# Optimization experiments

Hardware: AMD Instinct MI355X
Metric: run time of the kernel (lower is better)

The kernel has to match this reference:

```python
import jax, jax.numpy as jnp
import numpy as np

K_BITS = 8
QMAX = float(2 ** (K_BITS - 1) - 1)  # 127 for symmetric int8 fake quant
BN_EPS = 1e-5
RES_SCALE = 1.0


def _ste(v, q):
    # straight-through estimator: forward q, backward identity wrt v
    return v + jax.lax.stop_gradient(q - v)


def quant_act(x, alpha):
    # PAMS-style: clamp to learnable alpha, symmetric uniform fake-quant
    xc = jnp.clip(x, -alpha, alpha)
    scale = alpha / QMAX
    q = jnp.round(xc / scale) * scale
    return _ste(xc, q)


def quant_weight(w):
    # symmetric max-abs weight fake-quant
    scale = jnp.max(jnp.abs(w)) / QMAX
    q = jnp.clip(jnp.round(w / scale), -QMAX, QMAX) * scale
    return _ste(w, q)


def conv3x3(x, w):
    return jax.lax.conv_general_dilated(
        x, w, window_strides=(1, 1), padding=[(1, 1), (1, 1)],
        dimension_numbers=("NCHW", "OIHW", "NCHW"))


def batchnorm(x, gamma, beta):
    # training-mode BN: biased batch statistics over (N, H, W)
    mean = jnp.mean(x, axis=(0, 2, 3), keepdims=True)
    var = jnp.var(x, axis=(0, 2, 3), keepdims=True)
    xhat = (x - mean) * jax.lax.rsqrt(var + BN_EPS)
    return xhat * gamma[None, :, None, None] + beta[None, :, None, None]


def prelu(x, a):
    return jnp.where(x >= 0, x, a * x)


def setup_inputs() -> dict:
    key = jax.random.key(0)
    ks = jax.random.split(key, 4)
    C = 64
    identity = jax.random.normal(ks[0], (8, C, 192, 192), dtype=jnp.float32)
    # conv weights, default_init_weights scale 0.1 (kaiming-ish * 0.1)
    w1 = jax.random.normal(ks[1], (C, C, 3, 3), dtype=jnp.float32) * 0.1
    w2 = jax.random.normal(ks[2], (C, C, 3, 3), dtype=jnp.float32) * 0.1
    return {
        "identity": identity,
        "bits": jnp.ones((1,), jnp.float32),
        "f": jnp.ones((1,), jnp.float32),
        "bits_out": jnp.zeros((1,), jnp.float32),
        "w1": w1,
        "w2": w2,
        "alpha1": jnp.array(8.0, jnp.float32),
        "alpha2": jnp.array(8.0, jnp.float32),
        "gamma1": jnp.ones((C,), jnp.float32),
        "beta1": jnp.zeros((C,), jnp.float32),
        "gamma2": jnp.ones((C,), jnp.float32),
        "beta2": jnp.zeros((C,), jnp.float32),
        "prelu_a": jnp.array(0.25, jnp.float32),
        "shortcut": jnp.ones((1,), jnp.float32),
    }


def reference(identity, bits, f, bits_out, w1, w2, alpha1, alpha2,
              gamma1, beta1, gamma2, beta2, prelu_a, shortcut):
    # quant conv1: quantize input act + weights, 3x3 conv
    x = conv3x3(quant_act(identity, alpha1), quant_weight(w1))
    # PReLU then BN1 (module applies bn1(act(x)))
    x = batchnorm(prelu(x, prelu_a), gamma1, beta1)
    # quant conv2
    out = conv3x3(quant_act(x, alpha2), quant_weight(w2))
    out = batchnorm(out, gamma2, beta2)
    out = identity * shortcut + out * RES_SCALE
    return (out, bits, f, bits_out)
```

## Files before the change

kernel.cpp:

```cpp
#include <hip/hip_runtime.h>
#include <hip/hip_bf16.h>
#include <math.h>

#define CNUM   64
#define HH     192
#define WW     192
#define NBATCH 8
#define HWSZ   (HH * WW)
#define CHWSZ  (CNUM * HWSZ)
#define TOTALSZ ((size_t)NBATCH * CHWSZ)
#define QMAXF  127.0f
#define BNEPS  1e-5f
#define PW     194

typedef __attribute__((ext_vector_type(4))) int i32x4;

#define OFF_PK1    0
#define OFF_PK2    18432
#define OFF_STATS  36864
#define OFF_SUM1   36864
#define OFF_SSQ1   37120
#define OFF_SUM2   37376
#define OFF_SSQ2   37632
#define OFF_WMAX   37888
#define OFF_SW     37890
#define OFF_QA     38148
#define OFF_QB     (38148 + 9634816)

__device__ inline void gload16(const void* g, void* l) {
    __builtin_amdgcn_global_load_lds(
        (const __attribute__((address_space(1))) unsigned int*)g,
        (__attribute__((address_space(3))) unsigned int*)l, 16, 0, 0);
}
__device__ inline float bf2f(unsigned short u) {
    return __builtin_bit_cast(float, (unsigned)u << 16);
}

__global__ __launch_bounds__(256)
void wmax_kernel(const float* __restrict__ w1,
                 const float* __restrict__ w2,
                 unsigned* __restrict__ wmaxbits) {
    const int which = blockIdx.y;
    const float4* w4 = (const float4*)(which ? w2 : w1);
    const int b = (blockIdx.x * 256 + threadIdx.x) * 2;
    const float4 a = w4[b], c = w4[b + 1];
    float m = fmaxf(fmaxf(fmaxf(fabsf(a.x), fabsf(a.y)), fmaxf(fabsf(a.z), fabsf(a.w))),
                    fmaxf(fmaxf(fabsf(c.x), fabsf(c.y)), fmaxf(fabsf(c.z), fabsf(c.w))));
#pragma unroll
    for (int off = 1; off < 64; off <<= 1) m = fmaxf(m, __shfl_xor(m, off));
    if ((threadIdx.x & 63) == 0)
        atomicMax(wmaxbits + which, __builtin_bit_cast(unsigned, m));
}

__global__ __launch_bounds__(256)
void wpack_kernel(const float* __restrict__ w1,
                  const float* __restrict__ w2,
                  const unsigned* __restrict__ wmaxbits,
                  char* __restrict__ pk1,
                  char* __restrict__ pk2,
                  float* __restrict__ swout) {
    const int which = blockIdx.y;
    const float* w  = which ? w2 : w1;
    char*        pk = which ? pk2 : pk1;
    const float scale = __builtin_bit_cast(float, wmaxbits[which]) / QMAXF;
    if (blockIdx.x == 0 && threadIdx.x == 0) swout[which] = scale;
    const int i0 = (blockIdx.x * 256 + threadIdx.x) * 8;
#pragma unroll
    for (int k = 0; k < 8; ++k) {
        const int i = i0 + k;
        const int j   = i & 15;
        const int l   = (i >> 4) & 63;
        const int ocb = (i >> 10) & 3;
        const int t   = i >> 12;
        const int oc  = ocb * 16 + (l & 15);
        const int ic  = ((l >> 4) & 3) * 16 + j;
        float q = rintf(w[oc * 576 + ic * 9 + t] / scale);
        q = fminf(fmaxf(q, -QMAXF), QMAXF);
        pk[i] = (char)(int)q;
    }
}

__global__ __launch_bounds__(256)
void requant_kernel(const float* __restrict__ inp,
                    const float* __restrict__ alpha_p,
                    char* __restrict__ q) {
    const int tid  = threadIdx.x;
    const int xblk = blockIdx.x;
    const int py   = blockIdx.y;
    const int n    = blockIdx.z;
    char* qrow = q + ((size_t)n * PW + py) * (PW * 64);

    if (py == 0 || py == PW - 1) {
        for (int i = xblk * 256 + tid; i < PW * 4; i += 768)
            ((int4*)qrow)[i] = make_int4(0, 0, 0, 0);
        return;
    }
    if (xblk == 0 && tid < 4) ((int4*)qrow)[tid] = make_int4(0, 0, 0, 0);
    if (xblk == 2 && tid < 4) ((int4*)(qrow + 193 * 64))[tid] = make_int4(0, 0, 0, 0);

    const int gy = py - 1;
    const int x0 = xblk * 64;
    const float alpha  = alpha_p[0];
    const float inv_qs = QMAXF / alpha;

    __shared__ short s[64 * 72];
    const int xq  = tid & 15;
    const int icl = tid >> 4;

    float4 r[4];
#pragma unroll
    for (int p = 0; p < 4; ++p) {
        const int ic = icl * 4 + p;
        const size_t fo = ((size_t)n * CNUM + ic) * HWSZ + (size_t)gy * WW + x0 + xq * 4;
        r[p] = *(const float4*)(inp + fo);
    }
#pragma unroll
    for (int p = 0; p < 4; ++p) {
        const int ic = icl * 4 + p;
        float vv[4] = {r[p].x, r[p].y, r[p].z, r[p].w};
#pragma unroll
        for (int j = 0; j < 4; ++j) {
            float v = fminf(fmaxf(vv[j], -alpha), alpha);
            v = rintf(v * inv_qs);
            s[(xq * 4 + j) * 72 + ic] = (short)(int)v;
        }
    }
    __syncthreads();
    {
        const int xx = tid >> 2;
        const int g  = tid & 3;
        const int px = 1 + x0 + xx;
        const int gp = g ^ ((px >> 1) & 3);
        const short* sp = &s[xx * 72 + g * 16];
        int4 val;
        char* vb = (char*)&val;
#pragma unroll
        for (int j = 0; j < 16; ++j) vb[j] = (char)sp[j];
        *(int4*)(qrow + (size_t)px * 64 + gp * 16) = val;
    }
}

template<int XFORM, int SWZOUT>
__global__ __launch_bounds__(256, 3)
void conv_mfma_kernel(const char* __restrict__ q,
                      const char* __restrict__ wpk,
                      const float* __restrict__ swp,
                      const float* __restrict__ alpha_p,
                      const float* __restrict__ slope_p,
                      const float* __restrict__ st_sum,
                      const float* __restrict__ st_ssq,
                      const float* __restrict__ st_gamma,
                      const float* __restrict__ st_beta,
                      unsigned short* __restrict__ outp,
                      unsigned short* __restrict__ out_swz,
                      float* __restrict__ sum_g,
                      float* __restrict__ ssq_g) {
    __shared__ __align__(16) char s_in[1584 * 16];
    __shared__ __align__(16) short sT[SWZOUT ? 4 * 64 * 40 : 8];
    __shared__ float sred[256], ssred[256];
    __shared__ float sab[128];

    const int tid = threadIdx.x;
    const int x0 = blockIdx.x * 64;
    const int y0 = blockIdx.y * 4;
    const int n  = blockIdx.z;

    const float alpha  = alpha_p[0];
    const float inv_qs = QMAXF / alpha;

    if (XFORM) {
        if (tid < 64) {
            const float cnt = (float)(NBATCH * HWSZ);
            const float sm = st_sum[tid] + st_sum[64 + tid] + st_sum[128 + tid] + st_sum[192 + tid];
            const float sq = st_ssq[tid] + st_ssq[64 + tid] + st_ssq[128 + tid] + st_ssq[192 + tid];
            const float mean = sm / cnt;
            const float var  = sq / cnt - mean * mean;
            const float inv  = 1.0f / sqrtf(var + BNEPS);
            const float a = st_gamma[tid] * inv;
            sab[tid] = a;
            sab[64 + tid] = st_beta[tid] - mean * a;
        }
        __syncthreads();
        const unsigned short* qv = (const unsigned short*)q;
        const unsigned short* qb0 = qv + ((size_t)(n * PW + y0) * PW + x0) * 64;
#pragma unroll
        for (int k = 0; k < 7; ++k) {
            const int c = tid + k * 256;
            if (c < 1584) {
                const int r  = c / 264;
                const int w  = c - r * 264;
                const int x  = w >> 2, gp = w & 3;
                const int px = x0 + x, pyy = y0 + r;
                int4 val = make_int4(0, 0, 0, 0);
                if ((unsigned)(px - 1) < 192u && (unsigned)(pyy - 1) < 192u) {
                    const int g16 = gp ^ ((x >> 1) & 3);
                    const unsigned short* qp = qb0 + (size_t)r * (PW * 64) + (size_t)x * 64;
                    const int s0 = (2 * g16) ^ (px & 7);
                    const int4 v0 = *(const int4*)(qp + s0 * 8);
                    const int4 v1 = *(const int4*)(qp + (s0 ^ 1) * 8);
                    const unsigned short* u0 = (const unsigned short*)&v0;
                    const unsigned short* u1 = (const unsigned short*)&v1;
                    char vb[16];
#pragma unroll
                    for (int jj = 0; jj < 8; ++jj) {
                        const int ic = g16 * 16 + jj;
                        float xx0 = sab[ic] * bf2f(u0[jj]) + sab[64 + ic];
                        xx0 = fminf(fmaxf(xx0, -alpha), alpha);
                        vb[jj] = (char)(int)rintf(xx0 * inv_qs);
                    }
#pragma unroll
                    for (int jj = 0; jj < 8; ++jj) {
                        const int ic = g16 * 16 + 8 + jj;
                        float xx1 = sab[ic] * bf2f(u1[jj]) + sab[64 + ic];
                        xx1 = fminf(fmaxf(xx1, -alpha), alpha);
                        vb[8 + jj] = (char)(int)rintf(xx1 * inv_qs);
                    }
                    val = *(int4*)vb;
                }
                *(int4*)&s_in[c * 16] = val;
            }
        }
    } else {
        const char* g0 = q + ((size_t)(n * PW + y0) * PW + x0) * 64;
        for (int c = tid; c < 1584; c += 256) {
            const int r = c / 264;
            const int w = c - r * 264;
            gload16(g0 + (size_t)r * (PW * 64) + w * 16, &s_in[c * 16]);
        }
    }
    __syncthreads();

    const int wave  = tid >> 6;
    const int lane  = tid & 63;
    const int xlane = lane & 15;
    const int icgl  = lane >> 4;

    i32x4 acc[4][4];
#pragma unroll
    for (int m = 0; m < 4; ++m)
#pragma unroll
        for (int nb = 0; nb < 4; ++nb) acc[m][nb] = (i32x4){0, 0, 0, 0};

#pragma unroll
    for (int t = 0; t < 9; ++t) {
        const int ky = t / 3, kx = t % 3;
        const int r = wave + ky;
        i32x4 bfrag[4], afrag[4];
        const char* bp = wpk + ((size_t)(t * 4) * 64 + lane) * 16;
#pragma unroll
        for (int nb = 0; nb < 4; ++nb) bfrag[nb] = *(const i32x4*)(bp + (size_t)nb * 1024);
#pragma unroll
        for (int m = 0; m < 4; ++m) {
            const int x = m * 16 + xlane + kx;
            afrag[m] = *(const i32x4*)&s_in[(size_t)((r * 66 + x) * 4 + (icgl ^ ((x >> 1) & 3))) * 16];
        }
#pragma unroll
        for (int m = 0; m < 4; ++m)
#pragma unroll
            for (int nb = 0; nb < 4; ++nb)
                acc[m][nb] = __builtin_amdgcn_mfma_i32_16x16x64_i8(
                    afrag[m], bfrag[nb], acc[m][nb], 0, 0, 0);
    }

    const float sfin  = (alpha / QMAXF) * swp[0];
    const float slope = slope_p ? slope_p[0] : 1.0f;
    const int gy  = y0 + wave;
    const int gx0 = x0 + icgl * 4;

    if (SWZOUT) {
#pragma unroll
        for (int h = 0; h < 2; ++h) {
#pragma unroll
            for (int nbi = 0; nbi < 2; ++nbi) {
                const int nb = 2 * h + nbi;
                const int oc = nb * 16 + xlane;
                float s = 0.0f, ss = 0.0f;
#pragma unroll
                for (int m = 0; m < 4; ++m) {
#pragma unroll
                    for (int rgi = 0; rgi < 4; ++rgi) {
                        float a = (float)acc[m][nb][rgi] * sfin;
                        a = (a >= 0.0f) ? a : slope * a;
                        s += a;
                        ss += a * a;
                        const int pxl = m * 16 + icgl * 4 + rgi;
                        sT[(wave * 64 + pxl) * 40 + (nbi * 16 + xlane)] =
                            (short)__builtin_bit_cast(unsigned short, __float2bfloat16(a));
                    }
                }
                s  += __shfl_xor(s, 16);  s  += __shfl_xor(s, 32);
                ss += __shfl_xor(ss, 16); ss += __shfl_xor(ss, 32);
                if (icgl == 0) { sred[wave * 64 + oc] = s; ssred[wave * 64 + oc] = ss; }
            }
            __syncthreads();
            {
                const int py = gy + 1;
                unsigned short* qrow = out_swz + ((size_t)n * PW + py) * (PW * 64);
#pragma unroll
                for (int kk = 0; kk < 4; ++kk) {
                    const int idx = kk * 64 + lane;
                    const int xx  = idx >> 2;
                    const int gg  = idx & 3;
                    const int g8  = h * 4 + gg;
                    const int px  = x0 + 1 + xx;
                    const int slot = g8 ^ (px & 7);
                    *(int4*)(qrow + (size_t)px * 64 + slot * 8) =
                        *(const int4*)&sT[(wave * 64 + xx) * 40 + gg * 8];
                }
            }
            __syncthreads();
        }
    } else {
#pragma unroll
        for (int nb = 0; nb < 4; ++nb) {
            const int oc = nb * 16 + xlane;
            float s = 0.0f, ss = 0.0f;
#pragma unroll
            for (int m = 0; m < 4; ++m) {
                float v[4];
#pragma unroll
                for (int rgi = 0; rgi < 4; ++rgi) {
                    float a = (float)acc[m][nb][rgi] * sfin;
                    a = (a >= 0.0f) ? a : slope * a;
                    v[rgi] = a;
                    s += a;
                    ss += a * a;
                }
                ushort4 pk;
                pk.x = __builtin_bit_cast(unsigned short, __float2bfloat16(v[0]));
                pk.y = __builtin_bit_cast(unsigned short, __float2bfloat16(v[1]));
                pk.z = __builtin_bit_cast(unsigned short, __float2bfloat16(v[2]));
                pk.w = __builtin_bit_cast(unsigned short, __float2bfloat16(v[3]));
                *(ushort4*)&outp[(size_t)(n * CNUM + oc) * HWSZ + (size_t)gy * WW + gx0 + m * 16] = pk;
            }
            s  += __shfl_xor(s, 16);  s  += __shfl_xor(s, 32);
            ss += __shfl_xor(ss, 16); ss += __shfl_xor(ss, 32);
            if (icgl == 0) { sred[wave * 64 + oc] = s; ssred[wave * 64 + oc] = ss; }
        }
        __syncthreads();
    }

    const int bank = (blockIdx.y ^ blockIdx.z) & 3;
    if (tid < 64) {
        atomicAdd(sum_g + bank * 64 + tid,
                  sred[tid] + sred[64 + tid] + sred[128 + tid] + sred[192 + tid]);
    } else if (tid < 128) {
        const int c = tid - 64;
        atomicAdd(ssq_g + bank * 64 + c,
                  ssred[c] + ssred[64 + c] + ssred[128 + c] + ssred[192 + c]);
    }
}

__global__ __launch_bounds__(256)
void final_kernel(const float* __restrict__ identity,
                  const unsigned short* __restrict__ t2,
                  const float* __restrict__ st_sum,
                  const float* __restrict__ st_ssq,
                  const float* __restrict__ st_gamma,
                  const float* __restrict__ st_beta,
                  const float* __restrict__ shortcut_p,
                  const float* __restrict__ bits,
                  const float* __restrict__ f,
                  const float* __restrict__ bits_out,
                  float* __restrict__ out) {
    __shared__ float sab[128];
    if (threadIdx.x < 64) {
        const int c = threadIdx.x;
        const float cnt = (float)(NBATCH * HWSZ);
        const float sm = st_sum[c] + st_sum[64 + c] + st_sum[128 + c] + st_sum[192 + c];
        const float sq = st_ssq[c] + st_ssq[64 + c] + st_ssq[128 + c] + st_ssq[192 + c];
        const float mean = sm / cnt;
        const float var  = sq / cnt - mean * mean;
        const float inv  = 1.0f / sqrtf(var + BNEPS);
        const float a = st_gamma[c] * inv;
        sab[c] = a;
        sab[64 + c] = st_beta[c] - mean * a;
    }
    __syncthreads();

    const size_t base = (size_t)blockIdx.x * 1024;
    const int   cch  = (int)((base / (HWSZ / 4)) % CNUM);
    const float a  = sab[cch];
    const float bb = sab[64 + cch];
    const float sc = shortcut_p[0];

    float4  idv[4];
    ushort4 tv[4];
#pragma unroll
    for (int k = 0; k < 4; ++k) {
        const size_t i4 = base + (size_t)k * 256 + threadIdx.x;
        idv[k] = ((const float4*)identity)[i4];
        tv[k]  = ((const ushort4*)t2)[i4];
    }
#pragma unroll
    for (int k = 0; k < 4; ++k) {
        const size_t i4 = base + (size_t)k * 256 + threadIdx.x;
        float4 o;
        o.x = idv[k].x * sc + a * bf2f(tv[k].x) + bb;
        o.y = idv[k].y * sc + a * bf2f(tv[k].y) + bb;
        o.z = idv[k].z * sc + a * bf2f(tv[k].z) + bb;
        o.w = idv[k].w * sc + a * bf2f(tv[k].w) + bb;
        ((float4*)out)[i4] = o;
    }
    if (blockIdx.x == 0 && threadIdx.x == 0) {
        out[TOTALSZ + 0] = bits[0];
        out[TOTALSZ + 1] = f[0];
        out[TOTALSZ + 2] = bits_out[0];
    }
}

extern "C" void kernel_launch(void* const* d_in, const int* in_sizes, int n_in,
                              void* d_out, int out_size, void* d_ws, size_t ws_size,
                              hipStream_t stream) {
    const float* identity = (const float*)d_in[0];
    const float* bits     = (const float*)d_in[1];
    const float* f        = (const float*)d_in[2];
    const float* bits_out = (const float*)d_in[3];
    const float* w1       = (const float*)d_in[4];
    const float* w2       = (const float*)d_in[5];
    const float* alpha1   = (const float*)d_in[6];
    const float* alpha2   = (const float*)d_in[7];
    const float* gamma1   = (const float*)d_in[8];
    const float* beta1    = (const float*)d_in[9];
    const float* gamma2   = (const float*)d_in[10];
    const float* beta2    = (const float*)d_in[11];
    const float* prelu_a  = (const float*)d_in[12];
    const float* shortcut = (const float*)d_in[13];
    float* out = (float*)d_out;
    float* ws  = (float*)d_ws;

    char*     pk1   = (char*)(ws + OFF_PK1);
    char*     pk2   = (char*)(ws + OFF_PK2);
    float*    sum1  = ws + OFF_SUM1;
    float*    ssq1  = ws + OFF_SSQ1;
    float*    sum2  = ws + OFF_SUM2;
    float*    ssq2  = ws + OFF_SSQ2;
    unsigned* wmaxb = (unsigned*)(ws + OFF_WMAX);
    float*    sw    = ws + OFF_SW;
    char*           qa = (char*)(ws + OFF_QA);
    unsigned short* qb = (unsigned short*)(ws + OFF_QB);
    unsigned short* t2 = (unsigned short*)(ws + OFF_QA);

    hipMemsetAsync(ws + OFF_STATS, 0, 1026 * sizeof(float), stream);
    hipLaunchKernelGGL(wmax_kernel, dim3(18, 2), dim3(256), 0, stream, w1, w2, wmaxb);
    hipLaunchKernelGGL(requant_kernel, dim3(3, PW, NBATCH), dim3(256), 0, stream,
                       identity, alpha1, qa);
    hipLaunchKernelGGL(wpack_kernel, dim3(18, 2), dim3(256), 0, stream,
                       w1, w2, wmaxb, pk1, pk2, sw);
    hipLaunchKernelGGL((conv_mfma_kernel<0, 1>), dim3(3, HH / 4, NBATCH), dim3(256), 0, stream,
                       qa, pk1, sw + 0, alpha1, prelu_a,
                       (const float*)nullptr, (const float*)nullptr,
                       (const float*)nullptr, (const float*)nullptr,
                       (unsigned short*)nullptr, qb, sum1, ssq1);
    hipLaunchKernelGGL((conv_mfma_kernel<1, 0>), dim3(3, HH / 4, NBATCH), dim3(256), 0, stream,
                       (const char*)qb, pk2, sw + 1, alpha2, (const float*)nullptr,
                       sum1, ssq1, gamma1, beta1,
                       t2, (unsigned short*)nullptr, sum2, ssq2);
    hipLaunchKernelGGL(final_kernel, dim3((unsigned)(TOTALSZ / 4 / 1024)), dim3(256), 0, stream,
                       identity, t2, sum2, ssq2, gamma2, beta2,
                       shortcut, bits, f, bits_out, out);
}
```

Before: 250.9 us.

## Fuse input activation quantization into first conv tile load

Removes the separate requant kernel that wrote a padded int8 NHWC copy of the input. The first conv now reads fp32 NCHW input directly, clamps and rounds it, and packs int8 values into the swizzled shared tile, with halo and padding handled in place. This drops one kernel launch and one write-plus-read pass over the int8 buffer. In exchange, each conv block re-reads its halo rows from fp32, which costs about 1.5x re-read on 4-row tiles. The shared-memory stores are also scalar 4-byte writes instead of asynchronous global-to-LDS loads.

```diff
diff --git a/kernel.cpp b/kernel.cpp
--- a/kernel.cpp
+++ b/kernel.cpp
@@ -24,14 +24,9 @@
 #define OFF_SSQ2   37632
 #define OFF_WMAX   37888
 #define OFF_SW     37890
-#define OFF_QA     38148
+#define OFF_T2     38148
 #define OFF_QB     (38148 + 9634816)
 
-__device__ inline void gload16(const void* g, void* l) {
-    __builtin_amdgcn_global_load_lds(
-        (const __attribute__((address_space(1))) unsigned int*)g,
-        (__attribute__((address_space(3))) unsigned int*)l, 16, 0, 0);
-}
 __device__ inline float bf2f(unsigned short u) {
     return __builtin_bit_cast(float, (unsigned)u << 16);
 }
@@ -80,69 +75,9 @@
     }
 }
 
-__global__ __launch_bounds__(256)
-void requant_kernel(const float* __restrict__ inp,
-                    const float* __restrict__ alpha_p,
-                    char* __restrict__ q) {
-    const int tid  = threadIdx.x;
-    const int xblk = blockIdx.x;
-    const int py   = blockIdx.y;
-    const int n    = blockIdx.z;
-    char* qrow = q + ((size_t)n * PW + py) * (PW * 64);
-
-    if (py == 0 || py == PW - 1) {
-        for (int i = xblk * 256 + tid; i < PW * 4; i += 768)
-            ((int4*)qrow)[i] = make_int4(0, 0, 0, 0);
-        return;
-    }
-    if (xblk == 0 && tid < 4) ((int4*)qrow)[tid] = make_int4(0, 0, 0, 0);
-    if (xblk == 2 && tid < 4) ((int4*)(qrow + 193 * 64))[tid] = make_int4(0, 0, 0, 0);
-
-    const int gy = py - 1;
-    const int x0 = xblk * 64;
-    const float alpha  = alpha_p[0];
-    const float inv_qs = QMAXF / alpha;
-
-    __shared__ short s[64 * 72];
-    const int xq  = tid & 15;
-    const int icl = tid >> 4;
-
-    float4 r[4];
-#pragma unroll
-    for (int p = 0; p < 4; ++p) {
-        const int ic = icl * 4 + p;
-        const size_t fo = ((size_t)n * CNUM + ic) * HWSZ + (size_t)gy * WW + x0 + xq * 4;
-        r[p] = *(const float4*)(inp + fo);
-    }
-#pragma unroll
-    for (int p = 0; p < 4; ++p) {
-        const int ic = icl * 4 + p;
-        float vv[4] = {r[p].x, r[p].y, r[p].z, r[p].w};
-#pragma unroll
-        for (int j = 0; j < 4; ++j) {
-            float v = fminf(fmaxf(vv[j], -alpha), alpha);
-            v = rintf(v * inv_qs);
-            s[(xq * 4 + j) * 72 + ic] = (short)(int)v;
-        }
-    }
-    __syncthreads();
-    {
-        const int xx = tid >> 2;
-        const int g  = tid & 3;
-        const int px = 1 + x0 + xx;
-        const int gp = g ^ ((px >> 1) & 3);
-        const short* sp = &s[xx * 72 + g * 16];
-        int4 val;
-        char* vb = (char*)&val;
-#pragma unroll
-        for (int j = 0; j < 16; ++j) vb[j] = (char)sp[j];
-        *(int4*)(qrow + (size_t)px * 64 + gp * 16) = val;
-    }
-}
-
 template<int XFORM, int SWZOUT>
 __global__ __launch_bounds__(256, 3)
-void conv_mfma_kernel(const char* __restrict__ q,
+void conv_mfma_kernel(const void* __restrict__ in_p,
                       const char* __restrict__ wpk,
                       const float* __restrict__ swp,
                       const float* __restrict__ alpha_p,
@@ -158,7 +93,7 @@
     __shared__ __align__(16) char s_in[1584 * 16];
     __shared__ __align__(16) short sT[SWZOUT ? 4 * 64 * 40 : 8];
     __shared__ float sred[256], ssred[256];
-    __shared__ float sab[128];
+    __shared__ float sab[(XFORM == 1) ? 128 : 4];
 
     const int tid = threadIdx.x;
     const int x0 = blockIdx.x * 64;
@@ -168,7 +103,7 @@
     const float alpha  = alpha_p[0];
     const float inv_qs = QMAXF / alpha;
 
-    if (XFORM) {
+    if (XFORM == 1) {
         if (tid < 64) {
             const float cnt = (float)(NBATCH * HWSZ);
             const float sm = st_sum[tid] + st_sum[64 + tid] + st_sum[128 + tid] + st_sum[192 + tid];
@@ -181,7 +116,7 @@
             sab[64 + tid] = st_beta[tid] - mean * a;
         }
         __syncthreads();
-        const unsigned short* qv = (const unsigned short*)q;
+        const unsigned short* qv = (const unsigned short*)in_p;
         const unsigned short* qb0 = qv + ((size_t)(n * PW + y0) * PW + x0) * 64;
 #pragma unroll
         for (int k = 0; k < 7; ++k) {
@@ -221,11 +156,47 @@
             }
         }
     } else {
-        const char* g0 = q + ((size_t)(n * PW + y0) * PW + x0) * 64;
-        for (int c = tid; c < 1584; c += 256) {
-            const int r = c / 264;
-            const int w = c - r * 264;
-            gload16(g0 + (size_t)r * (PW * 64) + w * 16, &s_in[c * 16]);
+        const float* inp = (const float*)in_p;
+        const int xq  = tid & 15;
+        const int icl = tid >> 4;
+        const int g16 = icl >> 2;
+        const int wsl = (icl & 3) * 4;
+        const int nh  = (xq < 2) ? 2 : 1;
+        for (int r = 0; r < 6; ++r) {
+            const int gy = y0 - 1 + r;
+            const bool rv = ((unsigned)gy < 192u);
+            for (int half = 0; half < nh; ++half) {
+                const int qi  = half ? (16 + xq) : xq;
+                const int gxb = x0 - 4 + qi * 4;
+                const bool qv = rv && (gxb >= 0) && (gxb + 3 < 192);
+                float4 rr[4];
+                if (qv) {
+#pragma unroll
+                    for (int p = 0; p < 4; ++p) {
+                        const int ic = icl * 4 + p;
+                        rr[p] = *(const float4*)(inp + ((size_t)n * CNUM + ic) * HWSZ
+                                                 + (size_t)gy * WW + gxb);
+                    }
+                }
+#pragma unroll
+                for (int j = 0; j < 4; ++j) {
+                    const int xl = gxb + j + 1 - x0;
+                    if ((unsigned)xl <= 65u) {
+                        unsigned pkw = 0;
+                        if (qv) {
+#pragma unroll
+                            for (int p = 0; p < 4; ++p) {
+                                const float* rv4 = (const float*)&rr[p];
+                                float v = fminf(fmaxf(rv4[j], -alpha), alpha);
+                                v = rintf(v * inv_qs);
+                                pkw |= ((unsigned)(unsigned char)(char)(int)v) << (8 * p);
+                            }
+                        }
+                        const int gran = (r * 66 + xl) * 4 + (g16 ^ ((xl >> 1) & 3));
+                        *(unsigned*)&s_in[gran * 16 + wsl] = pkw;
+                    }
+                }
+            }
         }
     }
     __syncthreads();
@@ -437,23 +408,20 @@
     float*    ssq2  = ws + OFF_SSQ2;
     unsigned* wmaxb = (unsigned*)(ws + OFF_WMAX);
     float*    sw    = ws + OFF_SW;
-    char*           qa = (char*)(ws + OFF_QA);
     unsigned short* qb = (unsigned short*)(ws + OFF_QB);
-    unsigned short* t2 = (unsigned short*)(ws + OFF_QA);
+    unsigned short* t2 = (unsigned short*)(ws + OFF_T2);
 
     hipMemsetAsync(ws + OFF_STATS, 0, 1026 * sizeof(float), stream);
     hipLaunchKernelGGL(wmax_kernel, dim3(18, 2), dim3(256), 0, stream, w1, w2, wmaxb);
-    hipLaunchKernelGGL(requant_kernel, dim3(3, PW, NBATCH), dim3(256), 0, stream,
-                       identity, alpha1, qa);
     hipLaunchKernelGGL(wpack_kernel, dim3(18, 2), dim3(256), 0, stream,
                        w1, w2, wmaxb, pk1, pk2, sw);
-    hipLaunchKernelGGL((conv_mfma_kernel<0, 1>), dim3(3, HH / 4, NBATCH), dim3(256), 0, stream,
-                       qa, pk1, sw + 0, alpha1, prelu_a,
+    hipLaunchKernelGGL((conv_mfma_kernel<2, 1>), dim3(3, HH / 4, NBATCH), dim3(256), 0, stream,
+                       (const void*)identity, pk1, sw + 0, alpha1, prelu_a,
                        (const float*)nullptr, (const float*)nullptr,
                        (const float*)nullptr, (const float*)nullptr,
                        (unsigned short*)nullptr, qb, sum1, ssq1);
     hipLaunchKernelGGL((conv_mfma_kernel<1, 0>), dim3(3, HH / 4, NBATCH), dim3(256), 0, stream,
-                       (const char*)qb, pk2, sw + 1, alpha2, (const float*)nullptr,
+                       (const void*)qb, pk2, sw + 1, alpha2, (const float*)nullptr,
                        sum1, ssq1, gamma1, beta1,
                        t2, (unsigned short*)nullptr, sum2, ssq2);
     hipLaunchKernelGGL(final_kernel, dim3((unsigned)(TOTALSZ / 4 / 1024)), dim3(256), 0, stream,
```

Result: no change. 252.4 us (+0.6%).
